# Kernel tuning notes

Measured on AMD Instinct MI355X. Metric: run time of the kernel, lower is better.

## Reference

```python
import jax, jax.numpy as jnp
import numpy as np

T, B, I, H, O = 2048, 128, 32, 128, 1


def setup_inputs() -> dict:
    key = jax.random.key(0)
    ks = jax.random.split(key, 5)
    X = jax.random.normal(ks[0], (T, B, I), dtype=jnp.float32)
    W_in = jax.random.normal(ks[1], (H, I), dtype=jnp.float32) / np.sqrt(I)
    W_hh = jax.random.normal(ks[2], (H, H), dtype=jnp.float32) / np.sqrt(H)
    rnn_bias = jnp.zeros((H,), dtype=jnp.float32)
    alpha = jax.random.uniform(ks[3], (H,), dtype=jnp.float32)
    value_W = jax.random.normal(ks[4], (O, H), dtype=jnp.float32) / np.sqrt(H)
    value_bias = jnp.zeros((O,), dtype=jnp.float32)
    return {"X": X, "W_in": W_in, "W_hh": W_hh, "rnn_bias": rnn_bias,
            "alpha": alpha, "value_W": value_W, "value_bias": value_bias}


def reference(X, W_in, W_hh, rnn_bias, alpha, value_W, value_bias):
    # X: (T, B, I). Precompute input projections for all timesteps at once.
    xproj = jnp.einsum('tbi,hi->tbh', X, W_in)  # (T, B, H)

    def step(h_prev, xp_t):
        h_tilde = jnp.tanh(xp_t + h_prev @ W_hh.T + rnn_bias)
        h = (1.0 - alpha) * h_prev + alpha * h_tilde  # per-unit leaky blend
        return h, h

    h0 = jnp.zeros((X.shape[1], W_hh.shape[0]), dtype=X.dtype)
    last_hidden, Z = jax.lax.scan(step, h0, xproj)  # Z: (T, B, H)
    V = value_bias + jnp.einsum('tbh,oh->tbo', Z, value_W)  # (T, B, O)
    return V, last_hidden
```

## Files before the change

kernel.cpp:

```cpp
#include <hip/hip_runtime.h>

#define TT 2048
#define BB 128
#define II 32
#define HH 128
#define NW (TT / 8)

typedef float v2f __attribute__((ext_vector_type(2)));
typedef float v4f __attribute__((ext_vector_type(4)));
typedef unsigned int u32;
typedef __attribute__((address_space(3))) u32 lds_u32;
typedef const __attribute__((address_space(1))) u32 glb_u32;

__device__ __forceinline__ v2f pk_fma(v2f a, v2f b, v2f c) {
    v2f d;
    asm("v_pk_fma_f32 %0, %1, %2, %3" : "=v"(d) : "v"(a), "v"(b), "v"(c));
    return d;
}

template <int CTRL>
__device__ __forceinline__ float dpp_mov(float p) {
    return __int_as_float(__builtin_amdgcn_update_dpp(0, __float_as_int(p), CTRL, 0xF, 0xF, true));
}
template <int CTRL>
__device__ __forceinline__ float dpp_add(float p) {
    return p + dpp_mov<CTRL>(p);
}
template <int CTRL>
__device__ __forceinline__ float pair_red(float x, float y, bool sel) {
    float keep = sel ? y : x;
    float give = sel ? x : y;
    return keep + dpp_mov<CTRL>(give);
}

__global__ __launch_bounds__(256)
void vrnn_kernel(const float* __restrict__ X, const float* __restrict__ W_in,
                 const float* __restrict__ W_hh, const float* __restrict__ rnn_bias,
                 const float* __restrict__ alpha, const float* __restrict__ value_W,
                 const float* __restrict__ value_bias, float* __restrict__ out)
{
    const int b    = blockIdx.x;
    const int tid  = threadIdx.x;
    const int wave = tid >> 6;
    const int lane = tid & 63;
    const int g    = lane >> 4;
    const int j    = lane & 15;
    const int base = 32 * wave + 8 * g;
    const int rown = base + (j & 7);

    __shared__ __align__(16) float xw[2][8][II];
    __shared__ __align__(16) float hbuf[2][192];
    __shared__ __align__(16) float vres[TT];

    if (wave == 0) {
        const float* src = X + (size_t)(lane >> 3) * (BB * II) + b * II + (lane & 7) * 4;
        __builtin_amdgcn_global_load_lds((glb_u32*)src, (lds_u32*)(&xw[0][0][0]), 16, 0, 0);
    }

    const float SC = 2.8853900817779268f;

    v2f wh[8][4], wi8[8], binit[8];
#pragma unroll
    for (int r = 0; r < 8; ++r) {
        const float* wr = W_hh + (size_t)(base + r) * HH + 8 * j;
        v4f a0 = *(const v4f*)(wr);
        v4f a1 = *(const v4f*)(wr + 4);
        wh[r][0] = (v2f){a0.x * SC, a0.y * SC}; wh[r][1] = (v2f){a0.z * SC, a0.w * SC};
        wh[r][2] = (v2f){a1.x * SC, a1.y * SC}; wh[r][3] = (v2f){a1.z * SC, a1.w * SC};
        v2f wiv  = *(const v2f*)(W_in + (size_t)(base + r) * II + 2 * j);
        wi8[r]   = (v2f){wiv.x * SC, wiv.y * SC};
        binit[r] = (v2f){ (j == 0) ? rnn_bias[base + r] * SC : 0.0f, 0.0f };
    }
    v2f vwc[4];
#pragma unroll
    for (int i = 0; i < 4; ++i) vwc[i] = *(const v2f*)(value_W + 8 * j + 2 * i);
    const float al_own = alpha[rown];
    const float vb     = value_bias[0];
    const bool  b0 = (j & 1) != 0;
    const bool  b1 = (j & 2) != 0;
    const bool  b2 = (j & 4) != 0;
    const int   woff = 12 * (4 * wave + g) + (j & 7);
    float hreg = 0.0f;
    float hpre = 0.0f;
    v2f hpPrev[4] = { (v2f){0,0}, (v2f){0,0}, (v2f){0,0}, (v2f){0,0} };

    if (tid < 192) hbuf[1][tid] = 0.0f;
    __syncthreads();

    float* outV = out;
    float* outH = out + (size_t)TT * BB;

    for (int w = 0; w < NW; ++w) {
        if (wave == 0 && w + 1 < NW) {
            const float* src = X + (size_t)((w + 1) * 8 + (lane >> 3)) * (BB * II)
                                 + b * II + (lane & 7) * 4;
            __builtin_amdgcn_global_load_lds((glb_u32*)src,
                (lds_u32*)(&xw[(w + 1) & 1][0][0]), 16, 0, 0);
        }
#pragma unroll
        for (int s = 0; s < 8; ++s) {
            const int par = s & 1;
            const int t   = 8 * w + s;
            const float* hb = &hbuf[par ^ 1][12 * j];
            const v4f h0 = *(const v4f*)(hb);
            const v4f h1 = *(const v4f*)(hb + 4);
            const v2f xc = *(const v2f*)(&xw[w & 1][s][2 * j]);
            if (wave == ((s + 2) & 3) && t >= 2) {
                v2f vt = vwc[0] * hpPrev[0];
                vt = pk_fma(vwc[1], hpPrev[1], vt);
                vt = pk_fma(vwc[2], hpPrev[2], vt);
                vt = pk_fma(vwc[3], hpPrev[3], vt);
                float vs = vt.x + vt.y;
                vs = dpp_add<0xB1>(vs);
                vs = dpp_add<0x4E>(vs);
                const float uL = dpp_mov<0x104>(vs);
                const float uR = dpp_mov<0x114>(vs);
                vs += b2 ? uR : uL;
                vs = dpp_add<0x128>(vs);
                if (lane == 0) vres[t - 2] = vb + vs;
            }
            v2f hp[4] = { (v2f){h0.x, h0.y}, (v2f){h0.z, h0.w},
                          (v2f){h1.x, h1.y}, (v2f){h1.z, h1.w} };
            float p[8];
#pragma unroll
            for (int r = 0; r < 8; ++r) {
                v2f a = pk_fma(wi8[r], xc, binit[r]);
                a = pk_fma(wh[r][0], hp[0], a);
                a = pk_fma(wh[r][1], hp[1], a);
                a = pk_fma(wh[r][2], hp[2], a);
                a = pk_fma(wh[r][3], hp[3], a);
                p[r] = a.x + a.y;
            }
            float q0 = pair_red<0xB1>(p[0], p[1], b0);
            float q1 = pair_red<0xB1>(p[2], p[3], b0);
            float q2 = pair_red<0xB1>(p[4], p[5], b0);
            float q3 = pair_red<0xB1>(p[6], p[7], b0);
            float r0 = pair_red<0x4E>(q0, q1, b1);
            float r1 = pair_red<0x4E>(q2, q3, b1);
            const float k3  = b2 ? r1 : r0;
            const float g3  = b2 ? r0 : r1;
            const float vL  = dpp_mov<0x104>(g3);
            const float vR  = dpp_mov<0x114>(g3);
            float pre = k3 + (b2 ? vR : vL);
            pre += dpp_mov<0x128>(pre);
            const float e  = __builtin_amdgcn_exp2f(pre);
            const float rc = __builtin_amdgcn_rcpf(e + 1.0f);
            const float gt = fmaf(-2.0f, rc, 1.0f);
            hreg = fmaf(al_own, gt, hpre);
            hbuf[par][woff] = hreg;
            hpre = fmaf(-al_own, hreg, hreg);
            hpPrev[0] = hp[0]; hpPrev[1] = hp[1];
            hpPrev[2] = hp[2]; hpPrev[3] = hp[3];
            if (wave == 0 && s == 7)
                asm volatile("s_waitcnt vmcnt(0)" ::: "memory");
            asm volatile("s_waitcnt lgkmcnt(0)" ::: "memory");
            __builtin_amdgcn_s_barrier();
        }
    }

    if (wave == 0) {
        v2f vt = vwc[0] * hpPrev[0];
        vt = pk_fma(vwc[1], hpPrev[1], vt);
        vt = pk_fma(vwc[2], hpPrev[2], vt);
        vt = pk_fma(vwc[3], hpPrev[3], vt);
        float vs = vt.x + vt.y;
        vs = dpp_add<0xB1>(vs);
        vs = dpp_add<0x4E>(vs);
        float uL = dpp_mov<0x104>(vs);
        float uR = dpp_mov<0x114>(vs);
        vs += b2 ? uR : uL;
        vs = dpp_add<0x128>(vs);
        if (lane == 0) vres[TT - 2] = vb + vs;
    }
    if (wave == 1) {
        const float* hb = &hbuf[1][12 * j];
        const v4f h0 = *(const v4f*)(hb);
        const v4f h1 = *(const v4f*)(hb + 4);
        v2f hp[4] = { (v2f){h0.x, h0.y}, (v2f){h0.z, h0.w},
                      (v2f){h1.x, h1.y}, (v2f){h1.z, h1.w} };
        v2f vt = vwc[0] * hp[0];
        vt = pk_fma(vwc[1], hp[1], vt);
        vt = pk_fma(vwc[2], hp[2], vt);
        vt = pk_fma(vwc[3], hp[3], vt);
        float vs = vt.x + vt.y;
        vs = dpp_add<0xB1>(vs);
        vs = dpp_add<0x4E>(vs);
        float uL = dpp_mov<0x104>(vs);
        float uR = dpp_mov<0x114>(vs);
        vs += b2 ? uR : uL;
        vs = dpp_add<0x128>(vs);
        if (lane == 0) vres[TT - 1] = vb + vs;
    }
    if (j < 8)
        outH[(size_t)b * HH + base + j] = hreg;
    __syncthreads();
#pragma unroll
    for (int i = 0; i < TT / 256; ++i)
        outV[(size_t)(i * 256 + tid) * BB + b] = vres[i * 256 + tid];
}

extern "C" void kernel_launch(void* const* d_in, const int* in_sizes, int n_in,
                              void* d_out, int out_size, void* d_ws, size_t ws_size,
                              hipStream_t stream) {
    const float* X      = (const float*)d_in[0];
    const float* W_in   = (const float*)d_in[1];
    const float* W_hh   = (const float*)d_in[2];
    const float* rbias  = (const float*)d_in[3];
    const float* alpha  = (const float*)d_in[4];
    const float* vW     = (const float*)d_in[5];
    const float* vbias  = (const float*)d_in[6];
    float* out = (float*)d_out;

    vrnn_kernel<<<dim3(BB), dim3(256), 0, stream>>>(X, W_in, W_hh, rbias, alpha, vW, vbias, out);
}
```

Baseline: 807.4 us.

## Store hidden state in fp16 LDS and prefetch X into registers

The shared hidden-state exchange buffer now holds fp16 values instead of fp32, so each lane fetches its 8 hidden values with one 16-byte LDS read instead of two, and writes are halved. The X input is no longer staged in LDS through global_load_lds; each thread loads its own pair of X values for the next 8-step window into registers while the current window runs. The value-head dot product now uses the current step's loaded h instead of a copy from the previous step. Rounding h to fp16 on every step adds error that can accumulate through the recurrence across 2048 steps, and the extra X registers add register pressure.

```diff
diff --git a/kernel.cpp b/kernel.cpp
--- a/kernel.cpp
+++ b/kernel.cpp
@@ -1,4 +1,5 @@
 #include <hip/hip_runtime.h>
+#include <hip/hip_fp16.h>
 
 #define TT 2048
 #define BB 128
@@ -9,31 +10,30 @@
 typedef float v2f __attribute__((ext_vector_type(2)));
 typedef float v4f __attribute__((ext_vector_type(4)));
 typedef unsigned int u32;
-typedef __attribute__((address_space(3))) u32 lds_u32;
-typedef const __attribute__((address_space(1))) u32 glb_u32;
 
 __device__ __forceinline__ v2f pk_fma(v2f a, v2f b, v2f c) {
     v2f d;
     asm("v_pk_fma_f32 %0, %1, %2, %3" : "=v"(d) : "v"(a), "v"(b), "v"(c));
     return d;
 }
-
 template <int CTRL>
 __device__ __forceinline__ float dpp_mov(float p) {
     return __int_as_float(__builtin_amdgcn_update_dpp(0, __float_as_int(p), CTRL, 0xF, 0xF, true));
 }
 template <int CTRL>
-__device__ __forceinline__ float dpp_add(float p) {
-    return p + dpp_mov<CTRL>(p);
-}
+__device__ __forceinline__ float dpp_add(float p) { return p + dpp_mov<CTRL>(p); }
 template <int CTRL>
 __device__ __forceinline__ float pair_red(float x, float y, bool sel) {
     float keep = sel ? y : x;
     float give = sel ? x : y;
     return keep + dpp_mov<CTRL>(give);
 }
-
-__global__ __launch_bounds__(256)
+__device__ __forceinline__ void unpack2(u32 u, float& lo, float& hi) {
+    lo = __half2float(__ushort_as_half((unsigned short)u));
+    hi = __half2float(__ushort_as_half((unsigned short)(u >> 16)));
+}
+
+__global__ __launch_bounds__(256, 1)
 void vrnn_kernel(const float* __restrict__ X, const float* __restrict__ W_in,
                  const float* __restrict__ W_hh, const float* __restrict__ rnn_bias,
                  const float* __restrict__ alpha, const float* __restrict__ value_W,
@@ -48,14 +48,13 @@
     const int base = 32 * wave + 8 * g;
     const int rown = base + (j & 7);
 
-    __shared__ __align__(16) float xw[2][8][II];
-    __shared__ __align__(16) float hbuf[2][192];
-    __shared__ __align__(16) float vres[TT];
-
-    if (wave == 0) {
-        const float* src = X + (size_t)(lane >> 3) * (BB * II) + b * II + (lane & 7) * 4;
-        __builtin_amdgcn_global_load_lds((glb_u32*)src, (lds_u32*)(&xw[0][0][0]), 16, 0, 0);
-    }
+    __shared__ __align__(16) __half hbuf[2][160];
+    __shared__ __align__(16) float  vres[TT];
+
+    v2f xa[8], xb[8];
+#pragma unroll
+    for (int s = 0; s < 8; ++s)
+        xa[s] = *(const v2f*)(X + (size_t)s * (BB * II) + b * II + 2 * j);
 
     const float SC = 2.8853900817779268f;
 
@@ -79,105 +78,106 @@
     const bool  b0 = (j & 1) != 0;
     const bool  b1 = (j & 2) != 0;
     const bool  b2 = (j & 4) != 0;
-    const int   woff = 12 * (4 * wave + g) + (j & 7);
+    const int   roff_h = 8 * j + 16 * (j >> 3);
+    const int   woff_h = 8 * (rown >> 3) + 16 * (rown >> 6) + (rown & 7);
+
     float hreg = 0.0f;
     float hpre = 0.0f;
-    v2f hpPrev[4] = { (v2f){0,0}, (v2f){0,0}, (v2f){0,0}, (v2f){0,0} };
-
-    if (tid < 192) hbuf[1][tid] = 0.0f;
+
+    if (tid < 160) ((u32*)hbuf)[tid] = 0u;
     __syncthreads();
 
     float* outV = out;
     float* outH = out + (size_t)TT * BB;
 
-    for (int w = 0; w < NW; ++w) {
-        if (wave == 0 && w + 1 < NW) {
-            const float* src = X + (size_t)((w + 1) * 8 + (lane >> 3)) * (BB * II)
-                                 + b * II + (lane & 7) * 4;
-            __builtin_amdgcn_global_load_lds((glb_u32*)src,
-                (lds_u32*)(&xw[(w + 1) & 1][0][0]), 16, 0, 0);
+#define STEP(W_, S_, XARR)                                                     \
+    {                                                                          \
+        const int t   = 8 * (W_) + (S_);                                       \
+        const int par = (S_) & 1;                                              \
+        const __half* hb = &hbuf[par ^ 1][roff_h];                             \
+        const v4f hv = *(const v4f*)hb;                                        \
+        float h0, h1, h2, h3, h4, h5, h6, h7;                                  \
+        unpack2(__float_as_uint(hv.x), h0, h1);                                \
+        unpack2(__float_as_uint(hv.y), h2, h3);                                \
+        unpack2(__float_as_uint(hv.z), h4, h5);                                \
+        unpack2(__float_as_uint(hv.w), h6, h7);                                \
+        v2f hp[4] = { (v2f){h0, h1}, (v2f){h2, h3},                            \
+                      (v2f){h4, h5}, (v2f){h6, h7} };                          \
+        float p[8];                                                            \
+        _Pragma("unroll")                                                      \
+        for (int r = 0; r < 8; ++r) {                                          \
+            v2f a = pk_fma(wi8[r], XARR[S_], binit[r]);                        \
+            a = pk_fma(wh[r][0], hp[0], a);                                    \
+            a = pk_fma(wh[r][1], hp[1], a);                                    \
+            a = pk_fma(wh[r][2], hp[2], a);                                    \
+            a = pk_fma(wh[r][3], hp[3], a);                                    \
+            p[r] = a.x + a.y;                                                  \
+        }                                                                      \
+        float q0 = pair_red<0xB1>(p[0], p[1], b0);                             \
+        float q1 = pair_red<0xB1>(p[2], p[3], b0);                             \
+        float q2 = pair_red<0xB1>(p[4], p[5], b0);                             \
+        float q3 = pair_red<0xB1>(p[6], p[7], b0);                             \
+        float r0 = pair_red<0x4E>(q0, q1, b1);                                 \
+        float r1 = pair_red<0x4E>(q2, q3, b1);                                 \
+        const float k3 = b2 ? r1 : r0;                                         \
+        const float g3 = b2 ? r0 : r1;                                         \
+        const float vL = dpp_mov<0x104>(g3);                                   \
+        const float vR = dpp_mov<0x114>(g3);                                   \
+        float pre = k3 + (b2 ? vR : vL);                                       \
+        pre += dpp_mov<0x128>(pre);                                            \
+        const float e  = __builtin_amdgcn_exp2f(pre);                          \
+        const float rc = __builtin_amdgcn_rcpf(e + 1.0f);                      \
+        const float gt = fmaf(-2.0f, rc, 1.0f);                                \
+        hreg = fmaf(al_own, gt, hpre);                                         \
+        hbuf[par][woff_h] = __float2half(hreg);                                \
+        hpre = fmaf(-al_own, hreg, hreg);                                      \
+        if (wave == ((S_) & 3) && t > 0) {                                     \
+            v2f vt = vwc[0] * hp[0];                                           \
+            vt = pk_fma(vwc[1], hp[1], vt);                                    \
+            vt = pk_fma(vwc[2], hp[2], vt);                                    \
+            vt = pk_fma(vwc[3], hp[3], vt);                                    \
+            float vs = vt.x + vt.y;                                            \
+            vs = dpp_add<0xB1>(vs);                                            \
+            vs = dpp_add<0x4E>(vs);                                            \
+            const float uL = dpp_mov<0x104>(vs);                               \
+            const float uR = dpp_mov<0x114>(vs);                               \
+            vs += b2 ? uR : uL;                                                \
+            vs = dpp_add<0x128>(vs);                                           \
+            if (lane == 0) vres[t - 1] = vb + vs;                              \
+        }                                                                      \
+        asm volatile("s_waitcnt lgkmcnt(0)" ::: "memory");                     \
+        __builtin_amdgcn_s_barrier();                                          \
+    }
+
+    for (int w2 = 0; w2 < NW; w2 += 2) {
+#pragma unroll
+        for (int s = 0; s < 8; ++s) {
+            const int trow = 8 * (w2 + 1) + s;
+            xb[s] = *(const v2f*)(X + (size_t)trow * (BB * II) + b * II + 2 * j);
         }
 #pragma unroll
+        for (int s = 0; s < 8; ++s) STEP(w2, s, xa)
+#pragma unroll
         for (int s = 0; s < 8; ++s) {
-            const int par = s & 1;
-            const int t   = 8 * w + s;
-            const float* hb = &hbuf[par ^ 1][12 * j];
-            const v4f h0 = *(const v4f*)(hb);
-            const v4f h1 = *(const v4f*)(hb + 4);
-            const v2f xc = *(const v2f*)(&xw[w & 1][s][2 * j]);
-            if (wave == ((s + 2) & 3) && t >= 2) {
-                v2f vt = vwc[0] * hpPrev[0];
-                vt = pk_fma(vwc[1], hpPrev[1], vt);
-                vt = pk_fma(vwc[2], hpPrev[2], vt);
-                vt = pk_fma(vwc[3], hpPrev[3], vt);
-                float vs = vt.x + vt.y;
-                vs = dpp_add<0xB1>(vs);
-                vs = dpp_add<0x4E>(vs);
-                const float uL = dpp_mov<0x104>(vs);
-                const float uR = dpp_mov<0x114>(vs);
-                vs += b2 ? uR : uL;
-                vs = dpp_add<0x128>(vs);
-                if (lane == 0) vres[t - 2] = vb + vs;
-            }
-            v2f hp[4] = { (v2f){h0.x, h0.y}, (v2f){h0.z, h0.w},
-                          (v2f){h1.x, h1.y}, (v2f){h1.z, h1.w} };
-            float p[8];
-#pragma unroll
-            for (int r = 0; r < 8; ++r) {
-                v2f a = pk_fma(wi8[r], xc, binit[r]);
-                a = pk_fma(wh[r][0], hp[0], a);
-                a = pk_fma(wh[r][1], hp[1], a);
-                a = pk_fma(wh[r][2], hp[2], a);
-                a = pk_fma(wh[r][3], hp[3], a);
-                p[r] = a.x + a.y;
-            }
-            float q0 = pair_red<0xB1>(p[0], p[1], b0);
-            float q1 = pair_red<0xB1>(p[2], p[3], b0);
-            float q2 = pair_red<0xB1>(p[4], p[5], b0);
-            float q3 = pair_red<0xB1>(p[6], p[7], b0);
-            float r0 = pair_red<0x4E>(q0, q1, b1);
-            float r1 = pair_red<0x4E>(q2, q3, b1);
-            const float k3  = b2 ? r1 : r0;
-            const float g3  = b2 ? r0 : r1;
-            const float vL  = dpp_mov<0x104>(g3);
-            const float vR  = dpp_mov<0x114>(g3);
-            float pre = k3 + (b2 ? vR : vL);
-            pre += dpp_mov<0x128>(pre);
-            const float e  = __builtin_amdgcn_exp2f(pre);
-            const float rc = __builtin_amdgcn_rcpf(e + 1.0f);
-            const float gt = fmaf(-2.0f, rc, 1.0f);
-            hreg = fmaf(al_own, gt, hpre);
-            hbuf[par][woff] = hreg;
-            hpre = fmaf(-al_own, hreg, hreg);
-            hpPrev[0] = hp[0]; hpPrev[1] = hp[1];
-            hpPrev[2] = hp[2]; hpPrev[3] = hp[3];
-            if (wave == 0 && s == 7)
-                asm volatile("s_waitcnt vmcnt(0)" ::: "memory");
-            asm volatile("s_waitcnt lgkmcnt(0)" ::: "memory");
-            __builtin_amdgcn_s_barrier();
+            int trow = 8 * (w2 + 2) + s;
+            if (trow > TT - 1) trow = TT - 1;
+            xa[s] = *(const v2f*)(X + (size_t)trow * (BB * II) + b * II + 2 * j);
         }
-    }
+#pragma unroll
+        for (int s = 0; s < 8; ++s) STEP(w2 + 1, s, xb)
+    }
+#undef STEP
 
     if (wave == 0) {
-        v2f vt = vwc[0] * hpPrev[0];
-        vt = pk_fma(vwc[1], hpPrev[1], vt);
-        vt = pk_fma(vwc[2], hpPrev[2], vt);
-        vt = pk_fma(vwc[3], hpPrev[3], vt);
-        float vs = vt.x + vt.y;
-        vs = dpp_add<0xB1>(vs);
-        vs = dpp_add<0x4E>(vs);
-        float uL = dpp_mov<0x104>(vs);
-        float uR = dpp_mov<0x114>(vs);
-        vs += b2 ? uR : uL;
-        vs = dpp_add<0x128>(vs);
-        if (lane == 0) vres[TT - 2] = vb + vs;
-    }
-    if (wave == 1) {
-        const float* hb = &hbuf[1][12 * j];
-        const v4f h0 = *(const v4f*)(hb);
-        const v4f h1 = *(const v4f*)(hb + 4);
-        v2f hp[4] = { (v2f){h0.x, h0.y}, (v2f){h0.z, h0.w},
-                      (v2f){h1.x, h1.y}, (v2f){h1.z, h1.w} };
+        const __half* hb = &hbuf[1][roff_h];
+        const v4f hv = *(const v4f*)hb;
+        float h0, h1, h2, h3, h4, h5, h6, h7;
+        unpack2(__float_as_uint(hv.x), h0, h1);
+        unpack2(__float_as_uint(hv.y), h2, h3);
+        unpack2(__float_as_uint(hv.z), h4, h5);
+        unpack2(__float_as_uint(hv.w), h6, h7);
+        v2f hp[4] = { (v2f){h0, h1}, (v2f){h2, h3},
+                      (v2f){h4, h5}, (v2f){h6, h7} };
         v2f vt = vwc[0] * hp[0];
         vt = pk_fma(vwc[1], hp[1], vt);
         vt = pk_fma(vwc[2], hp[2], vt);
@@ -185,14 +185,14 @@
         float vs = vt.x + vt.y;
         vs = dpp_add<0xB1>(vs);
         vs = dpp_add<0x4E>(vs);
-        float uL = dpp_mov<0x104>(vs);
-        float uR = dpp_mov<0x114>(vs);
+        const float uL = dpp_mov<0x104>(vs);
+        const float uR = dpp_mov<0x114>(vs);
         vs += b2 ? uR : uL;
         vs = dpp_add<0x128>(vs);
         if (lane == 0) vres[TT - 1] = vb + vs;
     }
     if (j < 8)
-        outH[(size_t)b * HH + base + j] = hreg;
+        outH[(size_t)b * HH + rown] = hreg;
     __syncthreads();
 #pragma unroll
     for (int i = 0; i < TT / 256; ++i)
```

Result: slower. 830.7 us (+2.9%).
